# Performance work log

Measured on AMD Instinct MI355X. Metric: run time of the kernel, lower is better.

The kernel has to match this reference:

```python
import jax, jax.numpy as jnp
import numpy as np

B, T, D, N = 2, 2048, 2048, 16
H = D // N          # 128 head dim
F = H // 2          # 64 rotary frequencies


def setup_inputs() -> dict:
    key = jax.random.key(0)
    k1, k2, k3 = jax.random.split(key, 3)
    x = jax.random.normal(k1, (B, T, D), dtype=jnp.float32)
    # causal mask [T, T], True = attend
    mask = jnp.tril(jnp.ones((T, T), dtype=bool))
    # RoPE tables: freqs = 1 / 10000^(2i/H), angles = t * freqs
    freqs = 1.0 / (10000.0 ** (jnp.arange(0, H, 2, dtype=jnp.float32) / H))  # [F]
    angles = jnp.arange(T, dtype=jnp.float32)[:, None] * freqs[None, :]      # [T, F]
    cos, sin = jnp.cos(angles), jnp.sin(angles)
    w_attn = jax.random.normal(k2, (D, 3 * D), dtype=jnp.float32) * 0.02
    w_out = jax.random.normal(k3, (D, D), dtype=jnp.float32) * 0.02
    return {"x": x, "mask": mask, "cos": cos, "sin": sin,
            "w_attn": w_attn, "w_out": w_out}


def _rope(x_BNTH, cos_TF, sin_TF):
    # complex multiply on adjacent pairs of the head dim
    x = x_BNTH.reshape(*x_BNTH.shape[:-1], F, 2)  # [B,N,T,F,2]
    xr, xi = x[..., 0], x[..., 1]
    out_r = xr * cos_TF - xi * sin_TF             # broadcast [T,F] over [B,N,T,F]
    out_i = xr * sin_TF + xi * cos_TF
    return jnp.stack([out_r, out_i], axis=-1).reshape(x_BNTH.shape)


def reference(x, mask, cos, sin, w_attn, w_out):
    qkv = x @ w_attn                                  # [B,T,3D]
    q, k, v = jnp.split(qkv, 3, axis=-1)
    def to_heads(z):
        return z.reshape(B, T, N, H).transpose(0, 2, 1, 3)  # [B,N,T,H]
    q, k, v = to_heads(q), to_heads(k), to_heads(v)
    # NOTE: this module applies rotary embedding to k AND v (not q), per source
    k = _rope(k, cos, sin)
    v = _rope(v, cos, sin)
    scale = 1.0 / jnp.sqrt(jnp.asarray(H, dtype=q.dtype))
    scores = jnp.einsum('bnqh,bnkh->bnqk', q, k) * scale  # [B,N,T,T]
    scores = jnp.where(mask, scores, jnp.finfo(scores.dtype).min)
    attn = jax.nn.softmax(scores, axis=-1)
    o = jnp.einsum('bnqk,bnkh->bnqh', attn, v)            # [B,N,T,H]
    o = o.transpose(0, 2, 1, 3).reshape(B, T, D)          # [B,T,D]
    return o @ w_out
```

## Files before the change

### kernel.cpp

```cpp
#include <hip/hip_runtime.h>

typedef unsigned short u16;
typedef unsigned int u32;

#define B_ 2
#define T_ 2048
#define D_ 2048
#define N_ 16
#define H_ 128
#define F_ 64
#define QSCALE 0.12751743226f

typedef __attribute__((ext_vector_type(8))) __bf16 bf16x8;
typedef __attribute__((ext_vector_type(8))) short s16x8;
typedef __attribute__((ext_vector_type(4))) float f32x4;
typedef __attribute__((ext_vector_type(4))) u16 u16x4;
typedef __attribute__((ext_vector_type(4))) u32 u32x4;

__device__ inline u16 f2bf(float f) {
    union { float f; u32 u; } v; v.f = f;
    u32 u = v.u;
    u32 r = (u + 0x7FFFu + ((u >> 16) & 1u)) >> 16;
    return (u16)r;
}
__device__ inline float bf2f(u16 h) {
    union { u32 u; float f; } v; v.u = ((u32)h) << 16;
    return v.f;
}
__device__ inline bf16x8 ld8(const u16* p) {
    s16x8 r = *reinterpret_cast<const s16x8*>(p);
    return __builtin_bit_cast(bf16x8, r);
}
__device__ inline f32x4 mfma16(bf16x8 a, bf16x8 b, f32x4 c) {
    return __builtin_amdgcn_mfma_f32_16x16x32_bf16(a, b, c, 0, 0, 0);
}
__device__ inline void gload_lds16(const u16* g, u16* l) {
    __builtin_amdgcn_global_load_lds(
        (const __attribute__((address_space(1))) void*)g,
        (__attribute__((address_space(3))) void*)l, 16, 0, 0);
}
__device__ inline float exp2fast(float x) {
    float r;
    asm("v_exp_f32 %0, %1" : "=v"(r) : "v"(x));
    return r;
}
__device__ inline u32 cvtpk(float lo, float hi) {
    u32 r;
    asm("v_cvt_pk_bf16_f32 %0, %1, %2" : "=v"(r) : "v"(lo), "v"(hi));
    return r;
}

__global__ __launch_bounds__(256) void cvt_bf16(const float* __restrict__ in,
                                                u16* __restrict__ out, int n) {
    int i = (blockIdx.x * 256 + threadIdx.x) * 8;
    if (i >= n) return;
    float4 a = *reinterpret_cast<const float4*>(in + i);
    float4 b = *reinterpret_cast<const float4*>(in + i + 4);
    s16x8 o;
    o[0] = (short)f2bf(a.x); o[1] = (short)f2bf(a.y);
    o[2] = (short)f2bf(a.z); o[3] = (short)f2bf(a.w);
    o[4] = (short)f2bf(b.x); o[5] = (short)f2bf(b.y);
    o[6] = (short)f2bf(b.z); o[7] = (short)f2bf(b.w);
    *reinterpret_cast<s16x8*>(out + i) = o;
}

__global__ __launch_bounds__(256) void transpose_cvt(const float* __restrict__ in,
                                                     u16* __restrict__ out,
                                                     int K, int Nc) {
    __shared__ float tile[64][65];
    int n0 = blockIdx.x * 64, k0 = blockIdx.y * 64;
    int tid = threadIdx.x;
    int rr = tid >> 4;
    int cc = (tid & 15) * 4;
#pragma unroll
    for (int it = 0; it < 4; ++it) {
        int kk = it * 16 + rr;
        float4 v = *reinterpret_cast<const float4*>(in + (size_t)(k0 + kk) * Nc + n0 + cc);
        tile[kk][cc] = v.x; tile[kk][cc + 1] = v.y; tile[kk][cc + 2] = v.z; tile[kk][cc + 3] = v.w;
    }
    __syncthreads();
#pragma unroll
    for (int it = 0; it < 4; ++it) {
        int nn = it * 16 + rr;
        u16x4 o;
#pragma unroll
        for (int j = 0; j < 4; ++j) o[j] = f2bf(tile[cc + j][nn]);
        *reinterpret_cast<u16x4*>(out + (size_t)(n0 + nn) * K + k0 + cc) = o;
    }
}

#define BM 128
#define BN 128
#define BKg 32

__global__ __launch_bounds__(256) void gemm_bt(const u16* __restrict__ A,
                                               const u16* __restrict__ Bt,
                                               u16* __restrict__ Cb,
                                               float* __restrict__ Cf,
                                               int M, int Nn, int K, int out_f32) {
    __shared__ __align__(16) u16 As[2][BM * BKg];
    __shared__ __align__(16) u16 Bs[2][BM * BKg];
    const int tid = threadIdx.x;
    const int wave = tid >> 6, lane = tid & 63;
    const int m0 = blockIdx.y * BM, n0 = blockIdx.x * BN;
    const int lrow = lane >> 2, lcol = (lane & 3) * 8;
    const int wr = (wave >> 1) * 64, wc = (wave & 1) * 64;
    const int g = lane >> 4, c0 = lane & 15;

    f32x4 acc[4][4] = {};

    const int NT = K / BKg;

    auto stage = [&](int buf, int kt) {
        const int k0 = kt * BKg;
#pragma unroll
        for (int j = 0; j < 2; ++j) {
            const int c = wave + j * 4;
            gload_lds16(A + (size_t)(m0 + c * 16 + lrow) * K + k0 + lcol, &As[buf][c * 512]);
            gload_lds16(Bt + (size_t)(n0 + c * 16 + lrow) * K + k0 + lcol, &Bs[buf][c * 512]);
        }
    };

    stage(0, 0);
    __syncthreads();

    for (int t = 0; t < NT; ++t) {
        const int cur = t & 1;
        if (t + 1 < NT) stage(cur ^ 1, t + 1);
        bf16x8 af[4], bfr[4];
#pragma unroll
        for (int i = 0; i < 4; ++i) {
            af[i]  = ld8(&As[cur][(wr + i * 16 + c0) * BKg + g * 8]);
            bfr[i] = ld8(&Bs[cur][(wc + i * 16 + c0) * BKg + g * 8]);
        }
#pragma unroll
        for (int i = 0; i < 4; ++i)
#pragma unroll
            for (int j = 0; j < 4; ++j)
                acc[i][j] = mfma16(af[i], bfr[j], acc[i][j]);
        __syncthreads();
    }

#pragma unroll
    for (int i = 0; i < 4; ++i)
#pragma unroll
        for (int j = 0; j < 4; ++j)
#pragma unroll
            for (int r = 0; r < 4; ++r) {
                int row = m0 + wr + i * 16 + g * 4 + r;
                int col = n0 + wc + j * 16 + c0;
                float v = acc[i][j][r];
                if (out_f32) Cf[(size_t)row * Nn + col] = v;
                else         Cb[(size_t)row * Nn + col] = f2bf(v);
            }
}

__global__ __launch_bounds__(512, 2) void gemm256(const u16* __restrict__ A,
                                                  const u16* __restrict__ Bt,
                                                  u16* __restrict__ Cb,
                                                  float* __restrict__ Cf,
                                                  int M, int Nn, int K, int out_f32) {
    __shared__ __align__(16) u16 Asl[2][16384];
    __shared__ __align__(16) u16 Bsl[2][16384];
    const int tid = threadIdx.x;
    const int wave = tid >> 6, lane = tid & 63;
    const int wr = wave >> 2, wc = wave & 3;
    const int g = lane >> 4, c0 = lane & 15;

    const int bid = blockIdx.x;
    const int x = bid & 7;
    const int i = bid >> 3;
    const int m0 = (((x >> 2) * 8) + i / 6) << 8;
    const int n0 = (((x & 3) * 6) + (i % 6)) << 8;

    const int NT = K >> 6;

    const int jst = tid >> 3;
    const int ch = tid & 7;
    const int srcc = ch ^ (jst & 7);
    const int jA = jst + ((jst >> 5) * 96);
    const u16* Abase = A + (size_t)(m0 + jA) * K + srcc * 8;
    const u16* Bbase = Bt + (size_t)(n0 + jst) * K + srcc * 8;

    auto stageA = [&](int q, int kt) {
        gload_lds16(Abase + (size_t)(32 * q) * K + kt * 64,
                    &Asl[kt & 1][q * 4096 + tid * 8]);
    };
    auto stageB = [&](int b, int kt) {
        gload_lds16(Bbase + (size_t)(64 * b) * K + kt * 64,
                    &Bsl[kt & 1][b * 4096 + tid * 8]);
    };

#pragma unroll
    for (int q = 0; q < 4; ++q) { stageA(q, 0); stageB(q, 0); }
#pragma unroll
    for (int q = 0; q < 3; ++q) { stageA(q, 1); stageB(q, 1); }
    asm volatile("s_waitcnt vmcnt(6)" ::: "memory");
    __builtin_amdgcn_s_barrier();

    f32x4 acc[8][4] = {};
    bf16x8 bfr[4][2];

    for (int t = 0; t < NT; ++t) {
        const int cur = t & 1;
#pragma unroll
        for (int qd = 0; qd < 4; ++qd) {
            bf16x8 af[2][2];
            if (qd == 0) {
#pragma unroll
                for (int fj = 0; fj < 4; ++fj) {
                    const int br = wc * 64 + fj * 16 + c0;
#pragma unroll
                    for (int ks = 0; ks < 2; ++ks)
                        bfr[fj][ks] = ld8(&Bsl[cur][br * 64 + ((ks * 4 + g) ^ (br & 7)) * 8]);
                }
            }
#pragma unroll
            for (int u = 0; u < 2; ++u) {
                const int ar = qd * 64 + wr * 32 + u * 16 + c0;
#pragma unroll
                for (int ks = 0; ks < 2; ++ks)
                    af[u][ks] = ld8(&Asl[cur][ar * 64 + ((ks * 4 + g) ^ (ar & 7)) * 8]);
            }
            if (qd == 0) {
                if (t + 1 < NT) { stageA(3, t + 1); stageB(3, t + 1); }
            } else {
                if (t + 2 < NT) { stageA(qd - 1, t + 2); stageB(qd - 1, t + 2); }
            }
            if (qd == 0) asm volatile("s_waitcnt lgkmcnt(8)" ::: "memory");
            __builtin_amdgcn_s_barrier();
            asm volatile("s_waitcnt lgkmcnt(0)" ::: "memory");
            __builtin_amdgcn_s_setprio(1);
#pragma unroll
            for (int u = 0; u < 2; ++u)
#pragma unroll
                for (int fj = 0; fj < 4; ++fj)
#pragma unroll
                    for (int ks = 0; ks < 2; ++ks)
                        acc[qd * 2 + u][fj] = mfma16(af[u][ks], bfr[fj][ks], acc[qd * 2 + u][fj]);
            __builtin_amdgcn_s_setprio(0);
            if (qd == 3) {
                if (t + 2 < NT) asm volatile("s_waitcnt vmcnt(6)" ::: "memory");
                else            asm volatile("s_waitcnt vmcnt(0)" ::: "memory");
            }
            __builtin_amdgcn_s_barrier();
        }
    }

#pragma unroll
    for (int fi = 0; fi < 8; ++fi)
#pragma unroll
        for (int fj = 0; fj < 4; ++fj)
#pragma unroll
            for (int r = 0; r < 4; ++r) {
                int row = m0 + wr * 128 + fi * 16 + g * 4 + r;
                int col = n0 + wc * 64 + fj * 16 + c0;
                float v = acc[fi][fj][r];
                if (out_f32) Cf[(size_t)row * Nn + col] = v;
                else         Cb[(size_t)row * Nn + col] = f2bf(v);
            }
}

__global__ __launch_bounds__(256) void rope_split(const u16* __restrict__ qkv,
                                                  const float* __restrict__ cosT,
                                                  const float* __restrict__ sinT,
                                                  u16* __restrict__ qs,
                                                  u16* __restrict__ kr,
                                                  u16* __restrict__ vt) {
    __shared__ u16 vtile[64][129];
    int bi = blockIdx.x;
    int hn = bi >> 5;
    int tt = bi & 31;
    int b = hn >> 4, n = hn & 15;
    int t0 = tt * 64;
    int tid = threadIdx.x;
    int tl = tid >> 2;
    int h0 = (tid & 3) * 32;
    int t = t0 + tl;
    const u16* row = qkv + ((size_t)(b * T_ + t)) * (3 * D_);

#pragma unroll
    for (int u = 0; u < 4; ++u) {
        s16x8 raw = *reinterpret_cast<const s16x8*>(row + n * H_ + h0 + u * 8);
        s16x8 o;
#pragma unroll
        for (int e = 0; e < 8; ++e) o[e] = (short)f2bf(bf2f((u16)raw[e]) * QSCALE);
        *reinterpret_cast<s16x8*>(qs + ((size_t)hn * T_ + t) * H_ + h0 + u * 8) = o;
    }

    float cbuf[16], sbuf[16];
    const float* cr = cosT + (size_t)t * F_ + h0 / 2;
    const float* sr = sinT + (size_t)t * F_ + h0 / 2;
#pragma unroll
    for (int u = 0; u < 4; ++u) {
        float4 c4 = *reinterpret_cast<const float4*>(cr + u * 4);
        float4 s4 = *reinterpret_cast<const float4*>(sr + u * 4);
        cbuf[u * 4 + 0] = c4.x; cbuf[u * 4 + 1] = c4.y; cbuf[u * 4 + 2] = c4.z; cbuf[u * 4 + 3] = c4.w;
        sbuf[u * 4 + 0] = s4.x; sbuf[u * 4 + 1] = s4.y; sbuf[u * 4 + 2] = s4.z; sbuf[u * 4 + 3] = s4.w;
    }

#pragma unroll
    for (int u = 0; u < 4; ++u) {
        s16x8 raw = *reinterpret_cast<const s16x8*>(row + D_ + n * H_ + h0 + u * 8);
        s16x8 o;
#pragma unroll
        for (int p = 0; p < 4; ++p) {
            float xr = bf2f((u16)raw[2 * p]), xi = bf2f((u16)raw[2 * p + 1]);
            float cc = cbuf[u * 4 + p], ss = sbuf[u * 4 + p];
            o[2 * p]     = (short)f2bf(xr * cc - xi * ss);
            o[2 * p + 1] = (short)f2bf(xr * ss + xi * cc);
        }
        *reinterpret_cast<s16x8*>(kr + ((size_t)hn * T_ + t) * H_ + h0 + u * 8) = o;
    }

#pragma unroll
    for (int u = 0; u < 4; ++u) {
        s16x8 raw = *reinterpret_cast<const s16x8*>(row + 2 * D_ + n * H_ + h0 + u * 8);
#pragma unroll
        for (int p = 0; p < 4; ++p) {
            float xr = bf2f((u16)raw[2 * p]), xi = bf2f((u16)raw[2 * p + 1]);
            float cc = cbuf[u * 4 + p], ss = sbuf[u * 4 + p];
            vtile[tl][h0 + u * 8 + 2 * p]     = f2bf(xr * cc - xi * ss);
            vtile[tl][h0 + u * 8 + 2 * p + 1] = f2bf(xr * ss + xi * cc);
        }
    }
    __syncthreads();

    int hrow = tid >> 1;
    int th = (tid & 1) * 32;
    u16 tmp[32];
#pragma unroll
    for (int i = 0; i < 32; ++i) tmp[i] = vtile[th + i][hrow];
    u16* dst = vt + ((size_t)(hn * H_ + hrow)) * T_ + t0 + th;
#pragma unroll
    for (int u = 0; u < 4; ++u) {
        s16x8 o;
#pragma unroll
        for (int e = 0; e < 8; ++e) o[e] = (short)tmp[u * 8 + e];
        *reinterpret_cast<s16x8*>(dst + u * 8) = o;
    }
}

__global__ __launch_bounds__(256, 2) void attn_fwd(const u16* __restrict__ qs,
                                                   const u16* __restrict__ kr,
                                                   const u16* __restrict__ vt,
                                                   u16* __restrict__ ob) {
    __shared__ __align__(16) u16 Ks[2][8192];
    __shared__ __align__(16) u16 Vs[2][8192];

    const int wave = threadIdx.x >> 6, lane = threadIdx.x & 63;
    const int g = lane >> 4, c0 = lane & 15;

    const int wg = blockIdx.x;
    const int orig = (wg & 7) * 64 + (wg >> 3);
    const int hn = orig >> 4;
    const int qt = orig & 15;
    const int bq0 = (15 - qt) * 128;

    const u16* qh = qs + (size_t)hn * T_ * H_;
    const u16* kh = kr + (size_t)hn * T_ * H_;
    const u16* vh = vt + (size_t)hn * H_ * T_;

    const int q0[2] = { bq0 + wave * 16, bq0 + 64 + wave * 16 };

    bf16x8 qf[2][4];
#pragma unroll
    for (int i = 0; i < 2; ++i)
#pragma unroll
        for (int kf = 0; kf < 4; ++kf)
            qf[i][kf] = ld8(qh + (size_t)(q0[i] + c0) * H_ + kf * 32 + g * 8);

    f32x4 o[2][8] = {};
    float m[2] = { -1e30f, -1e30f };
    float l[2] = { 0.0f, 0.0f };

    const int nt = bq0 / 64 + 2;

    auto stage = [&](int buf, int t) {
        const int kv0 = t * 64;
#pragma unroll
        for (int j = 0; j < 4; ++j) {
            int ra = wave * 16 + j * 4 + (lane >> 4);
            int ca = ((lane & 15) * 8) ^ ((ra & 7) << 3);
            gload_lds16(kh + (size_t)(kv0 + ra) * H_ + ca, &Ks[buf][wave * 2048 + j * 512]);
            int rv = wave * 32 + j * 8 + (lane >> 3);
            int cv = ((lane & 7) * 8) ^ ((rv & 7) << 3);
            gload_lds16(vh + (size_t)rv * T_ + kv0 + cv, &Vs[buf][wave * 2048 + j * 512]);
        }
    };

    stage(0, 0);
    __syncthreads();

    const int srcA = ((g & 1) * 2) * 16 + c0;
    const int srcB = srcA + 16;
    const int sel  = g >> 1;

    for (int t = 0; t < nt; ++t) {
        const int cur = t & 1;
        const int kv0 = t * 64;
        if (t + 1 < nt) stage(cur ^ 1, t + 1);

        const bool a0 = kv0 < q0[0] + 16;
        const bool a1 = kv0 < q0[1] + 16;

        f32x4 s[2][4] = {};
        __builtin_amdgcn_s_setprio(1);
#pragma unroll
        for (int cc = 0; cc < 4; ++cc) {
            const int krow = cc * 16 + c0;
#pragma unroll
            for (int kf = 0; kf < 4; ++kf) {
                bf16x8 kfr = ld8(&Ks[cur][krow * 128 + ((kf * 32 + g * 8) ^ ((krow & 7) << 3))]);
                if (a0) s[0][cc] = mfma16(kfr, qf[0][kf], s[0][cc]);
                if (a1) s[1][cc] = mfma16(kfr, qf[1][kf], s[1][cc]);
            }
        }
        __builtin_amdgcn_s_setprio(0);

        bf16x8 pb[2][2];
#pragma unroll
        for (int i = 0; i < 2; ++i) {
            const bool act = i ? a1 : a0;
            if (!act) continue;
            const int qrow = q0[i] + c0;
            if (kv0 + 63 > q0[i]) {
#pragma unroll
                for (int cc = 0; cc < 4; ++cc) {
                    int kloc = kv0 + cc * 16 + g * 4;
#pragma unroll
                    for (int r = 0; r < 4; ++r)
                        if (kloc + r > qrow) s[i][cc][r] = -1e30f;
                }
            }
            float pmax = s[i][0][0];
#pragma unroll
            for (int cc = 0; cc < 4; ++cc)
#pragma unroll
                for (int r = 0; r < 4; ++r) pmax = fmaxf(pmax, s[i][cc][r]);
            if (!__all(pmax <= m[i] + 8.0f)) {
                pmax = fmaxf(pmax, __shfl_xor(pmax, 16));
                pmax = fmaxf(pmax, __shfl_xor(pmax, 32));
                float mn = fmaxf(m[i], pmax);
                float al = exp2fast(m[i] - mn);
                m[i] = mn;
                l[i] *= al;
#pragma unroll
                for (int hf = 0; hf < 8; ++hf)
#pragma unroll
                    for (int r = 0; r < 4; ++r) o[i][hf][r] *= al;
            }
            u32 w[4][2];
#pragma unroll
            for (int cc = 0; cc < 4; ++cc) {
                float p0 = exp2fast(s[i][cc][0] - m[i]);
                float p1 = exp2fast(s[i][cc][1] - m[i]);
                float p2 = exp2fast(s[i][cc][2] - m[i]);
                float p3 = exp2fast(s[i][cc][3] - m[i]);
                l[i] += (p0 + p1) + (p2 + p3);
                w[cc][0] = cvtpk(p0, p1);
                w[cc][1] = cvtpk(p2, p3);
            }
#pragma unroll
            for (int ks2 = 0; ks2 < 2; ++ks2) {
                u32 r00 = __shfl(w[ks2 * 2 + 0][0], srcA);
                u32 r01 = __shfl(w[ks2 * 2 + 0][1], srcA);
                u32 r02 = __shfl(w[ks2 * 2 + 0][0], srcB);
                u32 r03 = __shfl(w[ks2 * 2 + 0][1], srcB);
                u32 r10 = __shfl(w[ks2 * 2 + 1][0], srcA);
                u32 r11 = __shfl(w[ks2 * 2 + 1][1], srcA);
                u32 r12 = __shfl(w[ks2 * 2 + 1][0], srcB);
                u32 r13 = __shfl(w[ks2 * 2 + 1][1], srcB);
                u32x4 wv;
                wv[0] = sel ? r10 : r00;
                wv[1] = sel ? r11 : r01;
                wv[2] = sel ? r12 : r02;
                wv[3] = sel ? r13 : r03;
                pb[i][ks2] = __builtin_bit_cast(bf16x8, wv);
            }
        }

        __builtin_amdgcn_s_setprio(1);
#pragma unroll
        for (int hf = 0; hf < 8; ++hf) {
            const int vrow = hf * 16 + c0;
#pragma unroll
            for (int ks2 = 0; ks2 < 2; ++ks2) {
                bf16x8 vfr = ld8(&Vs[cur][vrow * 64 + ((ks2 * 32 + g * 8) ^ ((vrow & 7) << 3))]);
                if (a0) o[0][hf] = mfma16(vfr, pb[0][ks2], o[0][hf]);
                if (a1) o[1][hf] = mfma16(vfr, pb[1][ks2], o[1][hf]);
            }
        }
        __builtin_amdgcn_s_setprio(0);
        __syncthreads();
    }

    const int bb = hn >> 4, nn = hn & 15;
#pragma unroll
    for (int i = 0; i < 2; ++i) {
        float lt = l[i] + __shfl_xor(l[i], 16);
        lt += __shfl_xor(lt, 32);
        float inv = 1.0f / lt;
        const size_t rowoff = ((size_t)(bb * T_ + q0[i] + c0)) * D_ + nn * H_ + g * 4;
#pragma unroll
        for (int hf = 0; hf < 8; ++hf) {
            u16x4 pk;
#pragma unroll
            for (int r = 0; r < 4; ++r) pk[r] = f2bf(o[i][hf][r] * inv);
            *reinterpret_cast<u16x4*>(ob + rowoff + hf * 16) = pk;
        }
    }
}

extern "C" void kernel_launch(void* const* d_in, const int* in_sizes, int n_in,
                              void* d_out, int out_size, void* d_ws, size_t ws_size,
                              hipStream_t stream) {
    const float* x      = (const float*)d_in[0];
    const float* cosT   = (const float*)d_in[2];
    const float* sinT   = (const float*)d_in[3];
    const float* w_attn = (const float*)d_in[4];
    const float* w_out  = (const float*)d_in[5];
    float* out = (float*)d_out;

    char* ws = (char*)d_ws;
    u16* xb  = (u16*)(ws + 0);
    u16* wat = (u16*)(ws + 16777216);
    u16* wot = (u16*)(ws + 41943040);
    u16* qkv = (u16*)(ws + 50331648);
    u16* qsb = (u16*)(ws + 100663296);
    u16* krb = (u16*)(ws + 117440512);
    u16* vtb = (u16*)(ws + 134217728);
    u16* obf = (u16*)(ws + 0);

    cvt_bf16<<<(B_ * T_ * D_) / (256 * 8), 256, 0, stream>>>(x, xb, B_ * T_ * D_);
    transpose_cvt<<<dim3(3 * D_ / 64, D_ / 64), 256, 0, stream>>>(w_attn, wat, D_, 3 * D_);
    transpose_cvt<<<dim3(D_ / 64, D_ / 64), 256, 0, stream>>>(w_out, wot, D_, D_);
    gemm256<<<dim3((3 * D_ / 256) * (B_ * T_ / 256)), 512, 0, stream>>>(
        xb, wat, qkv, nullptr, B_ * T_, 3 * D_, D_, 0);
    rope_split<<<B_ * N_ * (T_ / 64), 256, 0, stream>>>(qkv, cosT, sinT, qsb, krb, vtb);
    attn_fwd<<<B_ * N_ * (T_ / 128), 256, 0, stream>>>(qsb, krb, vtb, obf);
    gemm_bt<<<dim3(D_ / BN, B_ * T_ / BM), 256, 0, stream>>>(obf, wot, nullptr, out,
                                                             B_ * T_, D_, D_, 1);
}
```

Baseline: 332.9 us.

## Software-pipeline LDS fragment reads one quad ahead in the bf16 GEMM

The GEMM main loop now loads the A fragments for the next row quad, and on the last quad the B fragments and first A fragments of the next K tile, right after issuing the current MFMAs. The fragments sit in double-buffered registers. This hides LDS read latency behind matrix math instead of stalling on lgkmcnt before each MFMA group. The global-load wait moves from quad 3 to quad 2 (vmcnt 4) so the next buffer is ready before the early reads. The cost is higher register pressure and tighter reasoning about buffer hazards.

```diff
diff --git a/kernel.cpp b/kernel.cpp
--- a/kernel.cpp
+++ b/kernel.cpp
@@ -191,43 +191,45 @@
                     &Bsl[kt & 1][b * 4096 + tid * 8]);
     };
 
+    bf16x8 afr[2][2][2];
+    bf16x8 bfr[4][2];
+
+    auto readB = [&](int bufi) {
+#pragma unroll
+        for (int fj = 0; fj < 4; ++fj) {
+            const int br = wc * 64 + fj * 16 + c0;
+#pragma unroll
+            for (int ks = 0; ks < 2; ++ks)
+                bfr[fj][ks] = ld8(&Bsl[bufi][br * 64 + ((ks * 4 + g) ^ (br & 7)) * 8]);
+        }
+    };
+
 #pragma unroll
     for (int q = 0; q < 4; ++q) { stageA(q, 0); stageB(q, 0); }
 #pragma unroll
     for (int q = 0; q < 3; ++q) { stageA(q, 1); stageB(q, 1); }
     asm volatile("s_waitcnt vmcnt(6)" ::: "memory");
     __builtin_amdgcn_s_barrier();
+    readB(0);
+#pragma unroll
+    for (int u = 0; u < 2; ++u) {
+        const int ar = wr * 32 + u * 16 + c0;
+#pragma unroll
+        for (int ks = 0; ks < 2; ++ks)
+            afr[0][u][ks] = ld8(&Asl[0][ar * 64 + ((ks * 4 + g) ^ (ar & 7)) * 8]);
+    }
 
     f32x4 acc[8][4] = {};
-    bf16x8 bfr[4][2];
 
     for (int t = 0; t < NT; ++t) {
         const int cur = t & 1;
 #pragma unroll
         for (int qd = 0; qd < 4; ++qd) {
-            bf16x8 af[2][2];
-            if (qd == 0) {
-#pragma unroll
-                for (int fj = 0; fj < 4; ++fj) {
-                    const int br = wc * 64 + fj * 16 + c0;
-#pragma unroll
-                    for (int ks = 0; ks < 2; ++ks)
-                        bfr[fj][ks] = ld8(&Bsl[cur][br * 64 + ((ks * 4 + g) ^ (br & 7)) * 8]);
-                }
-            }
-#pragma unroll
-            for (int u = 0; u < 2; ++u) {
-                const int ar = qd * 64 + wr * 32 + u * 16 + c0;
-#pragma unroll
-                for (int ks = 0; ks < 2; ++ks)
-                    af[u][ks] = ld8(&Asl[cur][ar * 64 + ((ks * 4 + g) ^ (ar & 7)) * 8]);
-            }
             if (qd == 0) {
                 if (t + 1 < NT) { stageA(3, t + 1); stageB(3, t + 1); }
             } else {
                 if (t + 2 < NT) { stageA(qd - 1, t + 2); stageB(qd - 1, t + 2); }
             }
-            if (qd == 0) asm volatile("s_waitcnt lgkmcnt(8)" ::: "memory");
             __builtin_amdgcn_s_barrier();
             asm volatile("s_waitcnt lgkmcnt(0)" ::: "memory");
             __builtin_amdgcn_s_setprio(1);
@@ -237,11 +239,32 @@
                 for (int fj = 0; fj < 4; ++fj)
 #pragma unroll
                     for (int ks = 0; ks < 2; ++ks)
-                        acc[qd * 2 + u][fj] = mfma16(af[u][ks], bfr[fj][ks], acc[qd * 2 + u][fj]);
+                        acc[qd * 2 + u][fj] =
+                            mfma16(afr[qd & 1][u][ks], bfr[fj][ks], acc[qd * 2 + u][fj]);
             __builtin_amdgcn_s_setprio(0);
-            if (qd == 3) {
-                if (t + 2 < NT) asm volatile("s_waitcnt vmcnt(6)" ::: "memory");
-                else            asm volatile("s_waitcnt vmcnt(0)" ::: "memory");
+            if (qd < 3) {
+#pragma unroll
+                for (int u = 0; u < 2; ++u) {
+                    const int ar = (qd + 1) * 64 + wr * 32 + u * 16 + c0;
+#pragma unroll
+                    for (int ks = 0; ks < 2; ++ks)
+                        afr[(qd + 1) & 1][u][ks] =
+                            ld8(&Asl[cur][ar * 64 + ((ks * 4 + g) ^ (ar & 7)) * 8]);
+                }
+            } else if (t + 1 < NT) {
+                readB(cur ^ 1);
+#pragma unroll
+                for (int u = 0; u < 2; ++u) {
+                    const int ar = wr * 32 + u * 16 + c0;
+#pragma unroll
+                    for (int ks = 0; ks < 2; ++ks)
+                        afr[0][u][ks] =
+                            ld8(&Asl[cur ^ 1][ar * 64 + ((ks * 4 + g) ^ (ar & 7)) * 8]);
+                }
+            }
+            if (qd == 2) {
+                if (t + 2 < NT)      asm volatile("s_waitcnt vmcnt(4)" ::: "memory");
+                else if (t + 1 < NT) asm volatile("s_waitcnt vmcnt(0)" ::: "memory");
             }
             __builtin_amdgcn_s_barrier();
         }
```

Measured after the change: 347.2 us. 1.04x slower.
